# Kernel optimization log

Measured on AMD Instinct MI355X. Metric: run time of the kernel, lower is better.

Reference implementation:

```python
import jax, jax.numpy as jnp
import numpy as np

B, C, H, W = 4, 256, 64, 64
HEADS, GROUPS = 8, 8
HEAD_DIM = C // HEADS
EPS_GN = 1e-5
EPS_NORM = 1e-12


def group_norm(x, gamma, beta):
    b, c, h, w = x.shape
    xr = x.reshape(b, GROUPS, c // GROUPS, h, w)
    mean = xr.mean(axis=(2, 3, 4), keepdims=True)
    var = xr.var(axis=(2, 3, 4), keepdims=True)
    xn = ((xr - mean) / jnp.sqrt(var + EPS_GN)).reshape(b, c, h, w)
    return xn * gamma[None, :, None, None] + beta[None, :, None, None]


def conv1x1(x, w):
    # w: (C_out, C_in) pointwise conv
    return jnp.einsum('oc,bchw->bohw', w, x)


def dwconv3x3(x, w, b):
    # depthwise 3x3, w: (C, 1, 3, 3)
    y = jax.lax.conv_general_dilated(
        x, w, window_strides=(1, 1), padding='SAME',
        dimension_numbers=('NCHW', 'OIHW', 'NCHW'),
        feature_group_count=C)
    return y + b[None, :, None, None]


def setup_inputs() -> dict:
    key = jax.random.key(0)
    ks = jax.random.split(key, 7)
    s = 0.05
    f32 = jnp.float32
    return {
        'x': jax.random.normal(ks[0], (B, C, H, W), f32),
        'wq': jax.random.normal(ks[1], (C, C), f32) * s,
        'gq_gamma': jnp.ones((C,), f32), 'gq_beta': jnp.zeros((C,), f32),
        'wk': jax.random.normal(ks[2], (C, C), f32) * s,
        'gk_gamma': jnp.ones((C,), f32), 'gk_beta': jnp.zeros((C,), f32),
        'wv': jax.random.normal(ks[3], (C, C), f32) * s,
        'wp': jax.random.normal(ks[4], (C, C), f32) * s,
        'bp': jnp.zeros((C,), f32),
        'gp_gamma': jnp.ones((C,), f32), 'gp_beta': jnp.zeros((C,), f32),
        'dw1': jax.random.normal(ks[5], (C, 1, 3, 3), f32) * s,
        'db1': jnp.zeros((C,), f32),
        'dw2': jax.random.normal(ks[6], (C, 1, 3, 3), f32) * s,
        'db2': jnp.zeros((C,), f32),
    }


def reference(x, wq, gq_gamma, gq_beta, wk, gk_gamma, gk_beta, wv,
              wp, bp, gp_gamma, gp_beta, dw1, db1, dw2, db2):
    b, c, h, w = x.shape
    q = group_norm(conv1x1(x, wq), gq_gamma, gq_beta)
    k = group_norm(conv1x1(x, wk), gk_gamma, gk_beta)
    v = conv1x1(x, wv)

    def to_tokens(t):
        # (B,C,H,W) -> (B*H*W, heads, head_dim)
        return t.transpose(0, 2, 3, 1).reshape(b * h * w, HEADS, HEAD_DIM)

    q, k, v = to_tokens(q), to_tokens(k), to_tokens(v)
    qn = q / jnp.maximum(jnp.linalg.norm(q, axis=-1, keepdims=True), EPS_NORM)
    kn = k / jnp.maximum(jnp.linalg.norm(k, axis=-1, keepdims=True), EPS_NORM)
    scale = 1.0 / np.sqrt(HEAD_DIM).astype(np.float32)
    # per-pixel spectral attention: (N, heads, d, d)
    attn = jnp.einsum('nhd,nhe->nhde', qn, kn) * scale
    attn = jax.nn.softmax(attn, axis=-1)
    out = jnp.einsum('nhde,nhe->nhd', attn, v)
    out = out.reshape(b, h, w, c).transpose(0, 3, 1, 2)

    pos = dwconv3x3(x, dw1, db1)
    pos = jax.nn.gelu(pos, approximate=False)
    pos = dwconv3x3(pos, dw2, db2)

    out = out + pos
    out = conv1x1(out, wp) + bp[None, :, None, None]
    out = group_norm(out, gp_gamma, gp_beta)
    return out
```

## Files before the change

### kernel.cpp

```cpp
#include <hip/hip_runtime.h>
#include <math.h>
#include <stdint.h>

#define C_ 256
#define HW_ 4096
#define PLANE (C_*HW_)
#define INV_CNT (1.f / 131072.f)
#define NSLOT 16

typedef __attribute__((ext_vector_type(8))) short bf16x8;
typedef __attribute__((ext_vector_type(4))) float f32x4;

__device__ __forceinline__ unsigned short f2bf(float f) {
    union { float f; unsigned int u; } v; v.f = f;
    unsigned int r = v.u + 0x7fffu + ((v.u >> 16) & 1u);
    return (unsigned short)(r >> 16);
}

__device__ __forceinline__ float bf2f(unsigned short u) {
    return __uint_as_float(((unsigned)u) << 16);
}

__device__ __forceinline__ void load_lds16(const void* g, void* l) {
    __builtin_amdgcn_global_load_lds(
        (const __attribute__((address_space(1))) unsigned int*)g,
        (__attribute__((address_space(3))) unsigned int*)l, 16, 0, 0);
}

__global__ __launch_bounds__(256) void transpose_cvt_kernel(
    const float* __restrict__ src, unsigned short* __restrict__ dst,
    const float* __restrict__ wq, const float* __restrict__ wk,
    const float* __restrict__ wv, const float* __restrict__ wp,
    unsigned short* __restrict__ wbf, float* __restrict__ stats)
{
    __shared__ float tile[64][65];
    int t = threadIdx.x;

    int bid = blockIdx.x + 64 * (blockIdx.y + 4 * blockIdx.z);
    {
        int widx = bid * 256 + t;
        const float* s = (widx < 65536) ? wq : (widx < 131072) ? wk
                       : (widx < 196608) ? wv : wp;
        wbf[widx] = f2bf(s[widx & 65535]);
        if (bid == 0) {
#pragma unroll
            for (int i = 0; i < 12; i++) stats[t + i * 256] = 0.f;
        }
    }

    int b = blockIdx.z;
    const float* s = src + (size_t)b * PLANE;
    unsigned short* d = dst + (size_t)b * PLANE;
    int c0 = blockIdx.y * 64, n0 = blockIdx.x * 64;
    int r = t >> 6, col = t & 63;
#pragma unroll
    for (int i = 0; i < 16; i++)
        tile[r + i * 4][col] = s[(size_t)(c0 + r + i * 4) * HW_ + n0 + col];
    __syncthreads();
#pragma unroll
    for (int i = 0; i < 16; i++)
        d[(size_t)(n0 + r + i * 4) * 256 + c0 + col] = f2bf(tile[col][r + i * 4]);
}

__global__ __launch_bounds__(256) void transpose_cvt_add_kernel(
    const unsigned short* __restrict__ pos, const unsigned short* __restrict__ attn,
    unsigned short* __restrict__ dst)
{
    __shared__ float tile[64][65];
    int b = blockIdx.z;
    const unsigned short* s = pos + (size_t)b * PLANE;
    const unsigned short* a = attn + (size_t)b * PLANE;
    unsigned short* d = dst + (size_t)b * PLANE;
    int c0 = blockIdx.y * 64, n0 = blockIdx.x * 64;
    int t = threadIdx.x;
    int r = t >> 6, col = t & 63;
#pragma unroll
    for (int i = 0; i < 16; i++)
        tile[r + i * 4][col] = bf2f(s[(size_t)(c0 + r + i * 4) * HW_ + n0 + col]);
    __syncthreads();
#pragma unroll
    for (int i = 0; i < 16; i++) {
        size_t o = (size_t)(n0 + r + i * 4) * 256 + c0 + col;
        d[o] = f2bf(tile[col][r + i * 4] + bf2f(a[o]));
    }
}

__device__ __forceinline__ void mfma_core(
    const unsigned short* __restrict__ A,
    const unsigned short* __restrict__ Bm,
    int m0, int n0, f32x4 (&acc)[4][4],
    unsigned short* sA, unsigned short* sB)
{
    const int t = threadIdx.x;
    const int lane = t & 63, wave = t >> 6;

#pragma unroll
    for (int i = 0; i < 4; i++)
#pragma unroll
        for (int j = 0; j < 4; j++) acc[i][j] = (f32x4)0.f;

    const int srow = wave * 32 + (lane >> 2);
    const int scol = (lane & 3) * 8;
    const unsigned short* ga = A  + (size_t)(m0 + srow) * 256 + scol;
    const unsigned short* gb = Bm + (size_t)(n0 + srow) * 256 + scol;
    const int lbase = (wave * 32) * 32;

    const int wm = wave >> 1, wn = wave & 1;
    const int fr = lane & 15, kg = lane >> 4;

    for (int k0 = 0; k0 < 256; k0 += 64) {
        if (k0) __syncthreads();
        load_lds16(ga + k0,            sA + lbase);
        load_lds16(ga + k0 + 16 * 256, sA + lbase + 16 * 32);
        load_lds16(gb + k0,            sB + lbase);
        load_lds16(gb + k0 + 16 * 256, sB + lbase + 16 * 32);
        load_lds16(ga + k0 + 32,            sA + 4096 + lbase);
        load_lds16(ga + k0 + 32 + 16 * 256, sA + 4096 + lbase + 16 * 32);
        load_lds16(gb + k0 + 32,            sB + 4096 + lbase);
        load_lds16(gb + k0 + 32 + 16 * 256, sB + 4096 + lbase + 16 * 32);
        __syncthreads();

#pragma unroll
        for (int kk = 0; kk < 2; kk++) {
            bf16x8 af[4], bfr[4];
#pragma unroll
            for (int i = 0; i < 4; i++) {
                af[i]  = *(const bf16x8*)(sA + kk * 4096 + (wm * 64 + i * 16 + fr) * 32 + kg * 8);
                bfr[i] = *(const bf16x8*)(sB + kk * 4096 + (wn * 64 + i * 16 + fr) * 32 + kg * 8);
            }
#pragma unroll
            for (int mi = 0; mi < 4; mi++)
#pragma unroll
                for (int ni = 0; ni < 4; ni++)
                    acc[mi][ni] = __builtin_amdgcn_mfma_f32_16x16x32_bf16(
                        af[mi], bfr[ni], acc[mi][ni], 0, 0, 0);
        }
    }
}

__device__ __forceinline__ void stat_atomic(
    float s0, float ss0, float s1, float ss1, float* d0, float* d1)
{
#pragma unroll
    for (int off = 32; off >= 1; off >>= 1) {
        s0  += __shfl_down(s0, off);  ss0 += __shfl_down(ss0, off);
        s1  += __shfl_down(s1, off);  ss1 += __shfl_down(ss1, off);
    }
    if ((threadIdx.x & 63) == 0) {
        atomicAdd(d0, s0); atomicAdd(d0 + 1, ss0);
        atomicAdd(d1, s1); atomicAdd(d1 + 1, ss1);
    }
}

__device__ __forceinline__ void stat_read(const float* sp, float& S, float& SS) {
    S = 0.f; SS = 0.f;
#pragma unroll
    for (int i = 0; i < NSLOT; i++) { S += sp[i * 2]; SS += sp[i * 2 + 1]; }
}

__device__ __forceinline__ float gelu_exact(float v) {
    return 0.5f * v * (1.f + erff(v * 0.70710678118654752f));
}

__global__ __launch_bounds__(256) void gemm_qkv_dw_kernel(
    const unsigned short* __restrict__ wbf, const unsigned short* __restrict__ xT,
    unsigned short* __restrict__ q, unsigned short* __restrict__ k,
    unsigned short* __restrict__ v, float* __restrict__ stats,
    const float* __restrict__ x,
    const float* __restrict__ dw1, const float* __restrict__ db1,
    const float* __restrict__ dw2, const float* __restrict__ db2,
    unsigned short* __restrict__ pos)
{
    __shared__ __align__(16) char smem[66 * 68 * 4 * 2];
    const int bid = blockIdx.x;
    const int t = threadIdx.x;

    if (bid < 768) {
        unsigned short* sA = (unsigned short*)smem;
        unsigned short* sB = (unsigned short*)(smem + 16384);
        int z = bid >> 6, rr = bid & 63;
        int batch = z & 3, which = z >> 2;
        unsigned short* Y = ((which == 0) ? q : (which == 1) ? k : v)
                            + (size_t)batch * PLANE;
        const unsigned short* A  = wbf + which * 65536;
        const unsigned short* Bm = xT + (size_t)batch * PLANE;
        const int m0 = (rr & 1) * 128;
        const int n0 = (rr >> 1) * 128;

        f32x4 acc[4][4];
        mfma_core(A, Bm, m0, n0, acc, sA, sB);

        const int lane = t & 63, wave = t >> 6;
        const int wm = wave >> 1, wn = wave & 1;
        const int cl = lane & 15, qd = lane >> 4;

        if (which < 2) {
            float s[2] = {0.f, 0.f}, ss[2] = {0.f, 0.f};
#pragma unroll
            for (int mi = 0; mi < 4; mi++)
#pragma unroll
                for (int ni = 0; ni < 4; ni++)
#pragma unroll
                    for (int r = 0; r < 4; r++) {
                        float vv = acc[mi][ni][r];
                        s[mi >> 1] += vv; ss[mi >> 1] += vv * vv;
                    }
            int g0 = (m0 >> 5) + wm * 2;
            int slot = (rr >> 1) & (NSLOT - 1);
            float* d0 = stats + (size_t)(which * 32 + batch * 8 + g0) * (NSLOT * 2) + slot * 2;
            stat_atomic(s[0], ss[0], s[1], ss[1], d0, d0 + NSLOT * 2);
        }

#pragma unroll
        for (int mi = 0; mi < 4; mi++) {
            int oc = m0 + wm * 64 + mi * 16 + qd * 4;
#pragma unroll
            for (int ni = 0; ni < 4; ni++) {
                int token = n0 + wn * 64 + ni * 16 + cl;
                uint2 pk;
                pk.x = (unsigned)f2bf(acc[mi][ni][0]) | ((unsigned)f2bf(acc[mi][ni][1]) << 16);
                pk.y = (unsigned)f2bf(acc[mi][ni][2]) | ((unsigned)f2bf(acc[mi][ni][3]) << 16);
                *(uint2*)&Y[(size_t)token * 256 + oc] = pk;
            }
        }
    } else {
        float* xs = (float*)smem;
        float* ps = xs + 66 * 68;
        const int bc = bid - 768;
        const int c = bc & 255;
        const float* plane = x + (size_t)bc * 4096;

        float w1[9], w2[9];
#pragma unroll
        for (int i = 0; i < 9; i++) { w1[i] = dw1[c * 9 + i]; w2[i] = dw2[c * 9 + i]; }
        const float b1 = db1[c], b2 = db2[c];

        for (int i = t; i < 66 * 66; i += 256) {
            int r = i / 66, cc = i - r * 66;
            int gr = r - 1, gc = cc - 1;
            float vv = 0.f;
            if ((unsigned)gr < 64u && (unsigned)gc < 64u) vv = plane[gr * 64 + gc];
            xs[r * 68 + cc] = vv;
        }
        __syncthreads();

        for (int i = t; i < 66 * 66; i += 256) {
            int pr = i / 66, pc = i - pr * 66;
            int gr = pr - 1, gc = pc - 1;
            float val = 0.f;
            if ((unsigned)gr < 64u && (unsigned)gc < 64u) {
                float s = b1;
#pragma unroll
                for (int ky = 0; ky < 3; ky++)
#pragma unroll
                    for (int kx = 0; kx < 3; kx++)
                        s += w1[ky * 3 + kx] * xs[(gr + ky) * 68 + (gc + kx)];
                val = gelu_exact(s);
            }
            ps[pr * 68 + pc] = val;
        }
        __syncthreads();

        for (int i = t; i < 4096; i += 256) {
            int orow = i >> 6, ocol = i & 63;
            float s = b2;
#pragma unroll
            for (int ky = 0; ky < 3; ky++)
#pragma unroll
                for (int kx = 0; kx < 3; kx++)
                    s += w2[ky * 3 + kx] * ps[(orow + ky) * 68 + (ocol + kx)];
            pos[(size_t)bc * 4096 + i] = f2bf(s);
        }
    }
}

__global__ __launch_bounds__(256) void gemm_out_mfma(
    const unsigned short* __restrict__ wbf, const unsigned short* __restrict__ aT,
    const float* __restrict__ bp, unsigned short* __restrict__ yb,
    float* __restrict__ stats)
{
    __shared__ __align__(16) unsigned short sA[2 * 128 * 32];
    __shared__ __align__(16) unsigned short sB[2 * 128 * 32];
    int batch = blockIdx.z;
    const unsigned short* A  = aT + (size_t)batch * PLANE;
    const unsigned short* Bm = wbf + 3 * 65536;
    unsigned short* Y = yb + (size_t)batch * PLANE;
    const int m0 = blockIdx.x * 128;
    const int n0 = blockIdx.y * 128;

    f32x4 acc[4][4];
    mfma_core(A, Bm, m0, n0, acc, sA, sB);

    const int lane = threadIdx.x & 63, wave = threadIdx.x >> 6;
    const int wm = wave >> 1, wn = wave & 1;
    const int cl = lane & 15, qd = lane >> 4;

    float s[2] = {0.f, 0.f}, ss[2] = {0.f, 0.f};
#pragma unroll
    for (int ni = 0; ni < 4; ni++) {
        int oc = n0 + wn * 64 + ni * 16 + cl;
        float bb = bp[oc];
#pragma unroll
        for (int mi = 0; mi < 4; mi++) {
            int tk = m0 + wm * 64 + mi * 16 + qd * 4;
            float4 o;
            o.x = acc[mi][ni][0] + bb; o.y = acc[mi][ni][1] + bb;
            o.z = acc[mi][ni][2] + bb; o.w = acc[mi][ni][3] + bb;
            s[ni >> 1] += o.x + o.y + o.z + o.w;
            ss[ni >> 1] += o.x * o.x + o.y * o.y + o.z * o.z + o.w * o.w;
            uint2 pk;
            pk.x = (unsigned)f2bf(o.x) | ((unsigned)f2bf(o.y) << 16);
            pk.y = (unsigned)f2bf(o.z) | ((unsigned)f2bf(o.w) << 16);
            *(uint2*)&Y[(size_t)oc * HW_ + tk] = pk;
        }
    }
    int g0 = (n0 >> 5) + wn * 2;
    int slot = blockIdx.x & (NSLOT - 1);
    float* d0 = stats + (size_t)(64 + batch * 8 + g0) * (NSLOT * 2) + slot * 2;
    stat_atomic(s[0], ss[0], s[1], ss[1], d0, d0 + NSLOT * 2);
}

__device__ __forceinline__ void bf16x32_load(const unsigned short* p, float* o) {
    const uint4* u4 = (const uint4*)p;
#pragma unroll
    for (int i = 0; i < 4; i++) {
        uint4 u = u4[i];
        o[i*8+0] = __uint_as_float(u.x << 16); o[i*8+1] = __uint_as_float(u.x & 0xffff0000u);
        o[i*8+2] = __uint_as_float(u.y << 16); o[i*8+3] = __uint_as_float(u.y & 0xffff0000u);
        o[i*8+4] = __uint_as_float(u.z << 16); o[i*8+5] = __uint_as_float(u.z & 0xffff0000u);
        o[i*8+6] = __uint_as_float(u.w << 16); o[i*8+7] = __uint_as_float(u.w & 0xffff0000u);
    }
}

__global__ __launch_bounds__(256) void attn_tok_kernel(
    const unsigned short* __restrict__ qtok, const unsigned short* __restrict__ ktok,
    const unsigned short* __restrict__ vtok, const float* __restrict__ stats,
    const float* __restrict__ gqg, const float* __restrict__ gqb,
    const float* __restrict__ gkg, const float* __restrict__ gkb,
    unsigned short* __restrict__ out)
{
    __shared__ float sqg[256], sqb[256], skg[256], skb[256];
    const int t = threadIdx.x;
    sqg[t] = gqg[t]; sqb[t] = gqb[t]; skg[t] = gkg[t]; skb[t] = gkb[t];
    __syncthreads();

    const int h = t & 7;
    const int pix = blockIdx.x * 32 + (t >> 3);
    const int b = pix >> 12;
    const size_t base = (size_t)pix * 256 + h * 32;
    const float K2 = 0.17677669529663687f * 1.4426950408889634f;

    float a[32], kn[32], vv[32];

    {
        float S, SS;
        stat_read(stats + (size_t)(b * 8 + h) * (NSLOT * 2), S, SS);
        float m = S * INV_CNT;
        float r = rsqrtf(SS * INV_CNT - m * m + 1e-5f);
        float qv[32], ssum = 0.f;
        bf16x32_load(qtok + base, qv);
#pragma unroll
        for (int j = 0; j < 32; j++) {
            float g = r * sqg[h * 32 + j];
            qv[j] = (qv[j] - m) * g + sqb[h * 32 + j];
            ssum = fmaf(qv[j], qv[j], ssum);
        }
        float inv = K2 / fmaxf(sqrtf(ssum), 1e-12f);
#pragma unroll
        for (int j = 0; j < 32; j++) a[j] = qv[j] * inv;
    }
    {
        float S, SS;
        stat_read(stats + (size_t)(32 + b * 8 + h) * (NSLOT * 2), S, SS);
        float m = S * INV_CNT;
        float r = rsqrtf(SS * INV_CNT - m * m + 1e-5f);
        float ssum = 0.f;
        bf16x32_load(ktok + base, kn);
#pragma unroll
        for (int j = 0; j < 32; j++) {
            float g = r * skg[h * 32 + j];
            kn[j] = (kn[j] - m) * g + skb[h * 32 + j];
            ssum = fmaf(kn[j], kn[j], ssum);
        }
        float inv = 1.f / fmaxf(sqrtf(ssum), 1e-12f);
#pragma unroll
        for (int j = 0; j < 32; j++) kn[j] *= inv;
    }
    bf16x32_load(vtok + base, vv);

    uint4* op = (uint4*)(out + base);
#pragma unroll
    for (int di = 0; di < 4; di++) {
        unsigned int od[4];
#pragma unroll
        for (int dp = 0; dp < 4; dp++) {
            float o2[2];
#pragma unroll
            for (int dd = 0; dd < 2; dd++) {
                float ad = a[di * 8 + dp * 2 + dd];
                float num = 0.f, den = 0.f;
#pragma unroll
                for (int e = 0; e < 32; e++) {
                    float w = __builtin_amdgcn_exp2f(ad * kn[e]);
                    num = fmaf(w, vv[e], num);
                    den += w;
                }
                o2[dd] = num / den;
            }
            od[dp] = (unsigned)f2bf(o2[0]) | ((unsigned)f2bf(o2[1]) << 16);
        }
        op[di] = make_uint4(od[0], od[1], od[2], od[3]);
    }
}

__global__ __launch_bounds__(256) void gn_apply_kernel(
    const unsigned short* __restrict__ src, float* __restrict__ y,
    const float* __restrict__ stats,
    const float* __restrict__ gamma, const float* __restrict__ beta)
{
    int i4 = blockIdx.x * 256 + threadIdx.x;
    int idx = i4 * 4;
    int c = (idx >> 12) & 255;
    int bg = ((idx >> 20) << 3) | (c >> 5);
    float S, SS;
    stat_read(stats + (size_t)(64 + bg) * (NSLOT * 2), S, SS);
    float mean = S * INV_CNT;
    float rstd = rsqrtf(SS * INV_CNT - mean * mean + 1e-5f);
    float ga = rstd * gamma[c], be = beta[c] - mean * ga;
    uint2 u = *(const uint2*)&src[idx];
    float4 v4;
    v4.x = bf2f((unsigned short)(u.x & 0xffff)) * ga + be;
    v4.y = bf2f((unsigned short)(u.x >> 16))    * ga + be;
    v4.z = bf2f((unsigned short)(u.y & 0xffff)) * ga + be;
    v4.w = bf2f((unsigned short)(u.y >> 16))    * ga + be;
    *(float4*)&y[idx] = v4;
}

extern "C" void kernel_launch(void* const* d_in, const int* in_sizes, int n_in,
                              void* d_out, int out_size, void* d_ws, size_t ws_size,
                              hipStream_t stream)
{
    const float* x   = (const float*)d_in[0];
    const float* wq  = (const float*)d_in[1];
    const float* gqg = (const float*)d_in[2];
    const float* gqb = (const float*)d_in[3];
    const float* wk  = (const float*)d_in[4];
    const float* gkg = (const float*)d_in[5];
    const float* gkb = (const float*)d_in[6];
    const float* wv  = (const float*)d_in[7];
    const float* wp  = (const float*)d_in[8];
    const float* bp  = (const float*)d_in[9];
    const float* gpg = (const float*)d_in[10];
    const float* gpb = (const float*)d_in[11];
    const float* dw1 = (const float*)d_in[12];
    const float* db1 = (const float*)d_in[13];
    const float* dw2 = (const float*)d_in[14];
    const float* db2 = (const float*)d_in[15];
    float* out = (float*)d_out;

    char* ws = (char*)d_ws;
    const size_t MB8 = (size_t)8 * 1024 * 1024;
    unsigned short* qtok = (unsigned short*)(ws);
    unsigned short* ktok = (unsigned short*)(ws + MB8);
    unsigned short* vtok = (unsigned short*)(ws + 2 * MB8);
    unsigned short* atok = (unsigned short*)(ws + 3 * MB8);
    unsigned short* xT   = (unsigned short*)(ws + 4 * MB8);
    unsigned short* aT   = xT;
    unsigned short* outb = ktok;
    unsigned short* wbf  = (unsigned short*)(ws + 5 * MB8);
    float*          stats= (float*)(ws + 5 * MB8 + 524288);
    unsigned short* pos  = (unsigned short*)(ws + 6 * MB8);

    dim3 blk(256);
    transpose_cvt_kernel<<<dim3(64, 4, 4), blk, 0, stream>>>(x, xT, wq, wk, wv, wp, wbf, stats);
    gemm_qkv_dw_kernel<<<dim3(1792), blk, 0, stream>>>(wbf, xT, qtok, ktok, vtok, stats,
                                                       x, dw1, db1, dw2, db2, pos);
    attn_tok_kernel<<<dim3(512), blk, 0, stream>>>(qtok, ktok, vtok, stats,
                                                   gqg, gqb, gkg, gkb, atok);
    transpose_cvt_add_kernel<<<dim3(64, 4, 4), blk, 0, stream>>>(pos, atok, aT);
    gemm_out_mfma<<<dim3(32, 2, 4), blk, 0, stream>>>(wbf, aT, bp, outb, stats);
    gn_apply_kernel<<<dim3(4096), blk, 0, stream>>>(outb, out, stats, gpg, gpb);
}
```

Before: 182.0 us.

## Fuse all stages into one cooperative persistent kernel with grid syncs

Replaces six separate kernel launches with a single cooperative persistent kernel that runs the weight conversion, transpose, depthwise conv, QKV GEMM, attention, output GEMM and group-norm apply as phases separated by grid.sync. The pos add is folded into the attention phase, which reads pos tiles through LDS, so the separate transpose-add pass and its intermediate buffer go away. The goal is to cut launch overhead and the extra memory round trips. In exchange, the grid is capped at a fixed occupancy-based size, grid-wide barriers are added, and the depthwise conv no longer overlaps with the QKV GEMM.

```diff
diff --git a/kernel.cpp b/kernel.cpp
--- a/kernel.cpp
+++ b/kernel.cpp
@@ -1,12 +1,16 @@
 #include <hip/hip_runtime.h>
+#include <hip/hip_cooperative_groups.h>
 #include <math.h>
 #include <stdint.h>
+
+namespace cg = cooperative_groups;
 
 #define C_ 256
 #define HW_ 4096
 #define PLANE (C_*HW_)
 #define INV_CNT (1.f / 131072.f)
 #define NSLOT 16
+#define PSTRIDE 264
 
 typedef __attribute__((ext_vector_type(8))) short bf16x8;
 typedef __attribute__((ext_vector_type(4))) float f32x4;
@@ -27,61 +31,15 @@
         (__attribute__((address_space(3))) unsigned int*)l, 16, 0, 0);
 }
 
-__global__ __launch_bounds__(256) void transpose_cvt_kernel(
-    const float* __restrict__ src, unsigned short* __restrict__ dst,
-    const float* __restrict__ wq, const float* __restrict__ wk,
-    const float* __restrict__ wv, const float* __restrict__ wp,
-    unsigned short* __restrict__ wbf, float* __restrict__ stats)
-{
-    __shared__ float tile[64][65];
-    int t = threadIdx.x;
-
-    int bid = blockIdx.x + 64 * (blockIdx.y + 4 * blockIdx.z);
-    {
-        int widx = bid * 256 + t;
-        const float* s = (widx < 65536) ? wq : (widx < 131072) ? wk
-                       : (widx < 196608) ? wv : wp;
-        wbf[widx] = f2bf(s[widx & 65535]);
-        if (bid == 0) {
-#pragma unroll
-            for (int i = 0; i < 12; i++) stats[t + i * 256] = 0.f;
-        }
-    }
-
-    int b = blockIdx.z;
-    const float* s = src + (size_t)b * PLANE;
-    unsigned short* d = dst + (size_t)b * PLANE;
-    int c0 = blockIdx.y * 64, n0 = blockIdx.x * 64;
-    int r = t >> 6, col = t & 63;
-#pragma unroll
-    for (int i = 0; i < 16; i++)
-        tile[r + i * 4][col] = s[(size_t)(c0 + r + i * 4) * HW_ + n0 + col];
-    __syncthreads();
-#pragma unroll
-    for (int i = 0; i < 16; i++)
-        d[(size_t)(n0 + r + i * 4) * 256 + c0 + col] = f2bf(tile[col][r + i * 4]);
-}
-
-__global__ __launch_bounds__(256) void transpose_cvt_add_kernel(
-    const unsigned short* __restrict__ pos, const unsigned short* __restrict__ attn,
-    unsigned short* __restrict__ dst)
-{
-    __shared__ float tile[64][65];
-    int b = blockIdx.z;
-    const unsigned short* s = pos + (size_t)b * PLANE;
-    const unsigned short* a = attn + (size_t)b * PLANE;
-    unsigned short* d = dst + (size_t)b * PLANE;
-    int c0 = blockIdx.y * 64, n0 = blockIdx.x * 64;
-    int t = threadIdx.x;
-    int r = t >> 6, col = t & 63;
-#pragma unroll
-    for (int i = 0; i < 16; i++)
-        tile[r + i * 4][col] = bf2f(s[(size_t)(c0 + r + i * 4) * HW_ + n0 + col]);
-    __syncthreads();
-#pragma unroll
-    for (int i = 0; i < 16; i++) {
-        size_t o = (size_t)(n0 + r + i * 4) * 256 + c0 + col;
-        d[o] = f2bf(tile[col][r + i * 4] + bf2f(a[o]));
+__device__ __forceinline__ void bf16x32_load(const unsigned short* p, float* o) {
+    const uint4* u4 = (const uint4*)p;
+#pragma unroll
+    for (int i = 0; i < 4; i++) {
+        uint4 u = u4[i];
+        o[i*8+0] = __uint_as_float(u.x << 16); o[i*8+1] = __uint_as_float(u.x & 0xffff0000u);
+        o[i*8+2] = __uint_as_float(u.y << 16); o[i*8+3] = __uint_as_float(u.y & 0xffff0000u);
+        o[i*8+4] = __uint_as_float(u.z << 16); o[i*8+5] = __uint_as_float(u.z & 0xffff0000u);
+        o[i*8+6] = __uint_as_float(u.w << 16); o[i*8+7] = __uint_as_float(u.w & 0xffff0000u);
     }
 }
 
@@ -162,322 +120,382 @@
     return 0.5f * v * (1.f + erff(v * 0.70710678118654752f));
 }
 
-__global__ __launch_bounds__(256) void gemm_qkv_dw_kernel(
-    const unsigned short* __restrict__ wbf, const unsigned short* __restrict__ xT,
-    unsigned short* __restrict__ q, unsigned short* __restrict__ k,
-    unsigned short* __restrict__ v, float* __restrict__ stats,
-    const float* __restrict__ x,
-    const float* __restrict__ dw1, const float* __restrict__ db1,
-    const float* __restrict__ dw2, const float* __restrict__ db2,
-    unsigned short* __restrict__ pos)
+struct MegaParams {
+    const float* x;
+    const float* wq; const float* wk; const float* wv; const float* wp;
+    const float* bp;
+    const float* gqg; const float* gqb; const float* gkg; const float* gkb;
+    const float* gpg; const float* gpb;
+    const float* dw1; const float* db1; const float* dw2; const float* db2;
+    unsigned short* xT;
+    unsigned short* wbf;
+    unsigned short* qtok; unsigned short* ktok; unsigned short* vtok;
+    unsigned short* pos;
+    float* stats;
+    float* out;
+};
+
+__global__ __launch_bounds__(256, 3) void mega_kernel(MegaParams P)
 {
     __shared__ __align__(16) char smem[66 * 68 * 4 * 2];
+    cg::grid_group grid = cg::this_grid();
     const int bid = blockIdx.x;
+    const int NBg = gridDim.x;
     const int t = threadIdx.x;
 
-    if (bid < 768) {
+    {
+        float (*tile)[65] = (float(*)[65])smem;
+        for (int u = bid; u < 1024; u += NBg) {
+            int widx = u * 256 + t;
+            const float* wsrc = (widx < 65536) ? P.wq : (widx < 131072) ? P.wk
+                              : (widx < 196608) ? P.wv : P.wp;
+            P.wbf[widx] = f2bf(wsrc[widx & 65535]);
+            if (u == 0) {
+#pragma unroll
+                for (int i = 0; i < 12; i++) P.stats[t + i * 256] = 0.f;
+            }
+            int b = u >> 8, c0 = ((u >> 6) & 3) * 64, n0 = (u & 63) * 64;
+            const float* s = P.x + (size_t)b * PLANE;
+            unsigned short* d = P.xT + (size_t)b * PLANE;
+            int r = t >> 6, col = t & 63;
+            __syncthreads();
+#pragma unroll
+            for (int i = 0; i < 16; i++)
+                tile[r + i * 4][col] = s[(size_t)(c0 + r + i * 4) * HW_ + n0 + col];
+            __syncthreads();
+#pragma unroll
+            for (int i = 0; i < 16; i++)
+                d[(size_t)(n0 + r + i * 4) * 256 + c0 + col] = f2bf(tile[col][r + i * 4]);
+        }
+    }
+
+    {
+        float* xs = (float*)smem;
+        float* ps = xs + 66 * 68;
+        for (int u = bid; u < 1024; u += NBg) {
+            int c = u & 255;
+            const float* plane = P.x + (size_t)u * 4096;
+            float w1[9], w2[9];
+#pragma unroll
+            for (int i = 0; i < 9; i++) { w1[i] = P.dw1[c * 9 + i]; w2[i] = P.dw2[c * 9 + i]; }
+            const float b1 = P.db1[c], b2 = P.db2[c];
+            __syncthreads();
+            for (int i = t; i < 66 * 66; i += 256) {
+                int r = i / 66, cc = i - r * 66;
+                int gr = r - 1, gc = cc - 1;
+                float v = 0.f;
+                if ((unsigned)gr < 64u && (unsigned)gc < 64u) v = plane[gr * 64 + gc];
+                xs[r * 68 + cc] = v;
+            }
+            __syncthreads();
+            for (int i = t; i < 66 * 66; i += 256) {
+                int pr = i / 66, pc = i - pr * 66;
+                int gr = pr - 1, gc = pc - 1;
+                float val = 0.f;
+                if ((unsigned)gr < 64u && (unsigned)gc < 64u) {
+                    float s = b1;
+#pragma unroll
+                    for (int ky = 0; ky < 3; ky++)
+#pragma unroll
+                        for (int kx = 0; kx < 3; kx++)
+                            s += w1[ky * 3 + kx] * xs[(gr + ky) * 68 + (gc + kx)];
+                    val = gelu_exact(s);
+                }
+                ps[pr * 68 + pc] = val;
+            }
+            __syncthreads();
+            for (int i = t; i < 4096; i += 256) {
+                int orow = i >> 6, ocol = i & 63;
+                float s = b2;
+#pragma unroll
+                for (int ky = 0; ky < 3; ky++)
+#pragma unroll
+                    for (int kx = 0; kx < 3; kx++)
+                        s += w2[ky * 3 + kx] * ps[(orow + ky) * 68 + (ocol + kx)];
+                P.pos[(size_t)u * 4096 + i] = f2bf(s);
+            }
+        }
+    }
+
+    grid.sync();
+
+    {
         unsigned short* sA = (unsigned short*)smem;
         unsigned short* sB = (unsigned short*)(smem + 16384);
-        int z = bid >> 6, rr = bid & 63;
-        int batch = z & 3, which = z >> 2;
-        unsigned short* Y = ((which == 0) ? q : (which == 1) ? k : v)
-                            + (size_t)batch * PLANE;
-        const unsigned short* A  = wbf + which * 65536;
-        const unsigned short* Bm = xT + (size_t)batch * PLANE;
-        const int m0 = (rr & 1) * 128;
-        const int n0 = (rr >> 1) * 128;
-
-        f32x4 acc[4][4];
-        mfma_core(A, Bm, m0, n0, acc, sA, sB);
-
-        const int lane = t & 63, wave = t >> 6;
-        const int wm = wave >> 1, wn = wave & 1;
-        const int cl = lane & 15, qd = lane >> 4;
-
-        if (which < 2) {
+        for (int u = bid; u < 768; u += NBg) {
+            int z = u >> 6, rr = u & 63;
+            int batch = z & 3, which = z >> 2;
+            unsigned short* Y = ((which == 0) ? P.qtok : (which == 1) ? P.ktok : P.vtok)
+                                + (size_t)batch * PLANE;
+            const unsigned short* A  = P.wbf + which * 65536;
+            const unsigned short* Bm = P.xT + (size_t)batch * PLANE;
+            const int m0 = (rr & 1) * 128;
+            const int n0 = (rr >> 1) * 128;
+
+            __syncthreads();
+            f32x4 acc[4][4];
+            mfma_core(A, Bm, m0, n0, acc, sA, sB);
+
+            const int lane = t & 63, wave = t >> 6;
+            const int wm = wave >> 1, wn = wave & 1;
+            const int cl = lane & 15, qd = lane >> 4;
+
+            if (which < 2) {
+                float s[2] = {0.f, 0.f}, ss[2] = {0.f, 0.f};
+#pragma unroll
+                for (int mi = 0; mi < 4; mi++)
+#pragma unroll
+                    for (int ni = 0; ni < 4; ni++)
+#pragma unroll
+                        for (int r = 0; r < 4; r++) {
+                            float vv = acc[mi][ni][r];
+                            s[mi >> 1] += vv; ss[mi >> 1] += vv * vv;
+                        }
+                int g0 = (m0 >> 5) + wm * 2;
+                int slot = (rr >> 1) & (NSLOT - 1);
+                float* d0 = P.stats + (size_t)(which * 32 + batch * 8 + g0) * (NSLOT * 2) + slot * 2;
+                stat_atomic(s[0], ss[0], s[1], ss[1], d0, d0 + NSLOT * 2);
+            }
+
+#pragma unroll
+            for (int mi = 0; mi < 4; mi++) {
+                int oc = m0 + wm * 64 + mi * 16 + qd * 4;
+#pragma unroll
+                for (int ni = 0; ni < 4; ni++) {
+                    int token = n0 + wn * 64 + ni * 16 + cl;
+                    uint2 pk;
+                    pk.x = (unsigned)f2bf(acc[mi][ni][0]) | ((unsigned)f2bf(acc[mi][ni][1]) << 16);
+                    pk.y = (unsigned)f2bf(acc[mi][ni][2]) | ((unsigned)f2bf(acc[mi][ni][3]) << 16);
+                    *(uint2*)&Y[(size_t)token * 256 + oc] = pk;
+                }
+            }
+        }
+    }
+
+    grid.sync();
+
+    {
+        float* sqg = (float*)smem;
+        float* sqb = sqg + 256;
+        float* skg = sqg + 512;
+        float* skb = sqg + 768;
+        unsigned short* ptile = (unsigned short*)(smem + 4096);
+        unsigned short* aT = P.xT;
+        sqg[t] = P.gqg[t]; sqb[t] = P.gqb[t]; skg[t] = P.gkg[t]; skb[t] = P.gkb[t];
+
+        const float K2 = 0.17677669529663687f * 1.4426950408889634f;
+        const int h = t & 7;
+        const int p = t >> 3;
+
+        for (int u = bid; u < 512; u += NBg) {
+            const int pix0 = u * 32;
+            const int b = pix0 >> 12;
+            const int n0 = pix0 & 4095;
+            __syncthreads();
+            {
+                const uint4* prow = (const uint4*)(P.pos + (size_t)b * PLANE + (size_t)t * HW_ + n0);
+#pragma unroll
+                for (int i = 0; i < 4; i++) {
+                    uint4 uu = prow[i];
+                    ptile[(i*8+0) * PSTRIDE + t] = (unsigned short)(uu.x & 0xffff);
+                    ptile[(i*8+1) * PSTRIDE + t] = (unsigned short)(uu.x >> 16);
+                    ptile[(i*8+2) * PSTRIDE + t] = (unsigned short)(uu.y & 0xffff);
+                    ptile[(i*8+3) * PSTRIDE + t] = (unsigned short)(uu.y >> 16);
+                    ptile[(i*8+4) * PSTRIDE + t] = (unsigned short)(uu.z & 0xffff);
+                    ptile[(i*8+5) * PSTRIDE + t] = (unsigned short)(uu.z >> 16);
+                    ptile[(i*8+6) * PSTRIDE + t] = (unsigned short)(uu.w & 0xffff);
+                    ptile[(i*8+7) * PSTRIDE + t] = (unsigned short)(uu.w >> 16);
+                }
+            }
+            __syncthreads();
+
+            const int pix = pix0 + p;
+            const size_t base = (size_t)pix * 256 + h * 32;
+            float a[32], kn[32], vv[32];
+
+            {
+                float S, SS;
+                stat_read(P.stats + (size_t)(b * 8 + h) * (NSLOT * 2), S, SS);
+                float m = S * INV_CNT;
+                float r = rsqrtf(SS * INV_CNT - m * m + 1e-5f);
+                float qv[32], ssum = 0.f;
+                bf16x32_load(P.qtok + base, qv);
+#pragma unroll
+                for (int j = 0; j < 32; j++) {
+                    float g = r * sqg[h * 32 + j];
+                    qv[j] = (qv[j] - m) * g + sqb[h * 32 + j];
+                    ssum = fmaf(qv[j], qv[j], ssum);
+                }
+                float inv = K2 / fmaxf(sqrtf(ssum), 1e-12f);
+#pragma unroll
+                for (int j = 0; j < 32; j++) a[j] = qv[j] * inv;
+            }
+            {
+                float S, SS;
+                stat_read(P.stats + (size_t)(32 + b * 8 + h) * (NSLOT * 2), S, SS);
+                float m = S * INV_CNT;
+                float r = rsqrtf(SS * INV_CNT - m * m + 1e-5f);
+                float ssum = 0.f;
+                bf16x32_load(P.ktok + base, kn);
+#pragma unroll
+                for (int j = 0; j < 32; j++) {
+                    float g = r * skg[h * 32 + j];
+                    kn[j] = (kn[j] - m) * g + skb[h * 32 + j];
+                    ssum = fmaf(kn[j], kn[j], ssum);
+                }
+                float inv = 1.f / fmaxf(sqrtf(ssum), 1e-12f);
+#pragma unroll
+                for (int j = 0; j < 32; j++) kn[j] *= inv;
+            }
+            bf16x32_load(P.vtok + base, vv);
+
+            const unsigned short* pl = ptile + p * PSTRIDE + h * 32;
+            uint4* op = (uint4*)(aT + base);
+#pragma unroll
+            for (int di = 0; di < 4; di++) {
+                uint4 up = *(const uint4*)(pl + di * 8);
+                float pv8[8];
+                pv8[0] = bf2f((unsigned short)(up.x & 0xffff)); pv8[1] = bf2f((unsigned short)(up.x >> 16));
+                pv8[2] = bf2f((unsigned short)(up.y & 0xffff)); pv8[3] = bf2f((unsigned short)(up.y >> 16));
+                pv8[4] = bf2f((unsigned short)(up.z & 0xffff)); pv8[5] = bf2f((unsigned short)(up.z >> 16));
+                pv8[6] = bf2f((unsigned short)(up.w & 0xffff)); pv8[7] = bf2f((unsigned short)(up.w >> 16));
+                unsigned int od[4];
+#pragma unroll
+                for (int dp = 0; dp < 4; dp++) {
+                    float o2[2];
+#pragma unroll
+                    for (int dd = 0; dd < 2; dd++) {
+                        float ad = a[di * 8 + dp * 2 + dd];
+                        float num = 0.f, den = 0.f;
+#pragma unroll
+                        for (int e = 0; e < 32; e++) {
+                            float w = __builtin_amdgcn_exp2f(ad * kn[e]);
+                            num = fmaf(w, vv[e], num);
+                            den += w;
+                        }
+                        o2[dd] = num / den + pv8[dp * 2 + dd];
+                    }
+                    od[dp] = (unsigned)f2bf(o2[0]) | ((unsigned)f2bf(o2[1]) << 16);
+                }
+                op[di] = make_uint4(od[0], od[1], od[2], od[3]);
+            }
+        }
+    }
+
+    grid.sync();
+
+    {
+        unsigned short* sA = (unsigned short*)smem;
+        unsigned short* sB = (unsigned short*)(smem + 16384);
+        const unsigned short* aT = P.xT;
+        unsigned short* outb = P.ktok;
+        for (int u = bid; u < 256; u += NBg) {
+            int bx = u & 31, z2 = u >> 5;
+            int ny = z2 & 1, batch = z2 >> 1;
+            const unsigned short* A  = aT + (size_t)batch * PLANE;
+            const unsigned short* Bm = P.wbf + 3 * 65536;
+            unsigned short* Y = outb + (size_t)batch * PLANE;
+            const int m0 = bx * 128;
+            const int n0 = ny * 128;
+
+            __syncthreads();
+            f32x4 acc[4][4];
+            mfma_core(A, Bm, m0, n0, acc, sA, sB);
+
+            const int lane = t & 63, wave = t >> 6;
+            const int wm = wave >> 1, wn = wave & 1;
+            const int cl = lane & 15, qd = lane >> 4;
+
             float s[2] = {0.f, 0.f}, ss[2] = {0.f, 0.f};
 #pragma unroll
-            for (int mi = 0; mi < 4; mi++)
-#pragma unroll
-                for (int ni = 0; ni < 4; ni++)
-#pragma unroll
-                    for (int r = 0; r < 4; r++) {
-                        float vv = acc[mi][ni][r];
-                        s[mi >> 1] += vv; ss[mi >> 1] += vv * vv;
-                    }
-            int g0 = (m0 >> 5) + wm * 2;
-            int slot = (rr >> 1) & (NSLOT - 1);
-            float* d0 = stats + (size_t)(which * 32 + batch * 8 + g0) * (NSLOT * 2) + slot * 2;
+            for (int ni = 0; ni < 4; ni++) {
+                int oc = n0 + wn * 64 + ni * 16 + cl;
+                float bb = P.bp[oc];
+#pragma unroll
+                for (int mi = 0; mi < 4; mi++) {
+                    int tk = m0 + wm * 64 + mi * 16 + qd * 4;
+                    float4 o;
+                    o.x = acc[mi][ni][0] + bb; o.y = acc[mi][ni][1] + bb;
+                    o.z = acc[mi][ni][2] + bb; o.w = acc[mi][ni][3] + bb;
+                    s[ni >> 1] += o.x + o.y + o.z + o.w;
+                    ss[ni >> 1] += o.x * o.x + o.y * o.y + o.z * o.z + o.w * o.w;
+                    uint2 pk;
+                    pk.x = (unsigned)f2bf(o.x) | ((unsigned)f2bf(o.y) << 16);
+                    pk.y = (unsigned)f2bf(o.z) | ((unsigned)f2bf(o.w) << 16);
+                    *(uint2*)&Y[(size_t)oc * HW_ + tk] = pk;
+                }
+            }
+            int g0 = (n0 >> 5) + wn * 2;
+            int slot = bx & (NSLOT - 1);
+            float* d0 = P.stats + (size_t)(64 + batch * 8 + g0) * (NSLOT * 2) + slot * 2;
             stat_atomic(s[0], ss[0], s[1], ss[1], d0, d0 + NSLOT * 2);
         }
-
-#pragma unroll
-        for (int mi = 0; mi < 4; mi++) {
-            int oc = m0 + wm * 64 + mi * 16 + qd * 4;
-#pragma unroll
-            for (int ni = 0; ni < 4; ni++) {
-                int token = n0 + wn * 64 + ni * 16 + cl;
-                uint2 pk;
-                pk.x = (unsigned)f2bf(acc[mi][ni][0]) | ((unsigned)f2bf(acc[mi][ni][1]) << 16);
-                pk.y = (unsigned)f2bf(acc[mi][ni][2]) | ((unsigned)f2bf(acc[mi][ni][3]) << 16);
-                *(uint2*)&Y[(size_t)token * 256 + oc] = pk;
-            }
-        }
-    } else {
-        float* xs = (float*)smem;
-        float* ps = xs + 66 * 68;
-        const int bc = bid - 768;
-        const int c = bc & 255;
-        const float* plane = x + (size_t)bc * 4096;
-
-        float w1[9], w2[9];
-#pragma unroll
-        for (int i = 0; i < 9; i++) { w1[i] = dw1[c * 9 + i]; w2[i] = dw2[c * 9 + i]; }
-        const float b1 = db1[c], b2 = db2[c];
-
-        for (int i = t; i < 66 * 66; i += 256) {
-            int r = i / 66, cc = i - r * 66;
-            int gr = r - 1, gc = cc - 1;
-            float vv = 0.f;
-            if ((unsigned)gr < 64u && (unsigned)gc < 64u) vv = plane[gr * 64 + gc];
-            xs[r * 68 + cc] = vv;
-        }
-        __syncthreads();
-
-        for (int i = t; i < 66 * 66; i += 256) {
-            int pr = i / 66, pc = i - pr * 66;
-            int gr = pr - 1, gc = pc - 1;
-            float val = 0.f;
-            if ((unsigned)gr < 64u && (unsigned)gc < 64u) {
-                float s = b1;
-#pragma unroll
-                for (int ky = 0; ky < 3; ky++)
-#pragma unroll
-                    for (int kx = 0; kx < 3; kx++)
-                        s += w1[ky * 3 + kx] * xs[(gr + ky) * 68 + (gc + kx)];
-                val = gelu_exact(s);
-            }
-            ps[pr * 68 + pc] = val;
-        }
-        __syncthreads();
-
-        for (int i = t; i < 4096; i += 256) {
-            int orow = i >> 6, ocol = i & 63;
-            float s = b2;
-#pragma unroll
-            for (int ky = 0; ky < 3; ky++)
-#pragma unroll
-                for (int kx = 0; kx < 3; kx++)
-                    s += w2[ky * 3 + kx] * ps[(orow + ky) * 68 + (ocol + kx)];
-            pos[(size_t)bc * 4096 + i] = f2bf(s);
-        }
-    }
-}
-
-__global__ __launch_bounds__(256) void gemm_out_mfma(
-    const unsigned short* __restrict__ wbf, const unsigned short* __restrict__ aT,
-    const float* __restrict__ bp, unsigned short* __restrict__ yb,
-    float* __restrict__ stats)
-{
-    __shared__ __align__(16) unsigned short sA[2 * 128 * 32];
-    __shared__ __align__(16) unsigned short sB[2 * 128 * 32];
-    int batch = blockIdx.z;
-    const unsigned short* A  = aT + (size_t)batch * PLANE;
-    const unsigned short* Bm = wbf + 3 * 65536;
-    unsigned short* Y = yb + (size_t)batch * PLANE;
-    const int m0 = blockIdx.x * 128;
-    const int n0 = blockIdx.y * 128;
-
-    f32x4 acc[4][4];
-    mfma_core(A, Bm, m0, n0, acc, sA, sB);
-
-    const int lane = threadIdx.x & 63, wave = threadIdx.x >> 6;
-    const int wm = wave >> 1, wn = wave & 1;
-    const int cl = lane & 15, qd = lane >> 4;
-
-    float s[2] = {0.f, 0.f}, ss[2] = {0.f, 0.f};
-#pragma unroll
-    for (int ni = 0; ni < 4; ni++) {
-        int oc = n0 + wn * 64 + ni * 16 + cl;
-        float bb = bp[oc];
-#pragma unroll
-        for (int mi = 0; mi < 4; mi++) {
-            int tk = m0 + wm * 64 + mi * 16 + qd * 4;
-            float4 o;
-            o.x = acc[mi][ni][0] + bb; o.y = acc[mi][ni][1] + bb;
-            o.z = acc[mi][ni][2] + bb; o.w = acc[mi][ni][3] + bb;
-            s[ni >> 1] += o.x + o.y + o.z + o.w;
-            ss[ni >> 1] += o.x * o.x + o.y * o.y + o.z * o.z + o.w * o.w;
-            uint2 pk;
-            pk.x = (unsigned)f2bf(o.x) | ((unsigned)f2bf(o.y) << 16);
-            pk.y = (unsigned)f2bf(o.z) | ((unsigned)f2bf(o.w) << 16);
-            *(uint2*)&Y[(size_t)oc * HW_ + tk] = pk;
-        }
-    }
-    int g0 = (n0 >> 5) + wn * 2;
-    int slot = blockIdx.x & (NSLOT - 1);
-    float* d0 = stats + (size_t)(64 + batch * 8 + g0) * (NSLOT * 2) + slot * 2;
-    stat_atomic(s[0], ss[0], s[1], ss[1], d0, d0 + NSLOT * 2);
-}
-
-__device__ __forceinline__ void bf16x32_load(const unsigned short* p, float* o) {
-    const uint4* u4 = (const uint4*)p;
-#pragma unroll
-    for (int i = 0; i < 4; i++) {
-        uint4 u = u4[i];
-        o[i*8+0] = __uint_as_float(u.x << 16); o[i*8+1] = __uint_as_float(u.x & 0xffff0000u);
-        o[i*8+2] = __uint_as_float(u.y << 16); o[i*8+3] = __uint_as_float(u.y & 0xffff0000u);
-        o[i*8+4] = __uint_as_float(u.z << 16); o[i*8+5] = __uint_as_float(u.z & 0xffff0000u);
-        o[i*8+6] = __uint_as_float(u.w << 16); o[i*8+7] = __uint_as_float(u.w & 0xffff0000u);
-    }
-}
-
-__global__ __launch_bounds__(256) void attn_tok_kernel(
-    const unsigned short* __restrict__ qtok, const unsigned short* __restrict__ ktok,
-    const unsigned short* __restrict__ vtok, const float* __restrict__ stats,
-    const float* __restrict__ gqg, const float* __restrict__ gqb,
-    const float* __restrict__ gkg, const float* __restrict__ gkb,
-    unsigned short* __restrict__ out)
-{
-    __shared__ float sqg[256], sqb[256], skg[256], skb[256];
-    const int t = threadIdx.x;
-    sqg[t] = gqg[t]; sqb[t] = gqb[t]; skg[t] = gkg[t]; skb[t] = gkb[t];
-    __syncthreads();
-
-    const int h = t & 7;
-    const int pix = blockIdx.x * 32 + (t >> 3);
-    const int b = pix >> 12;
-    const size_t base = (size_t)pix * 256 + h * 32;
-    const float K2 = 0.17677669529663687f * 1.4426950408889634f;
-
-    float a[32], kn[32], vv[32];
+    }
+
+    grid.sync();
 
     {
-        float S, SS;
-        stat_read(stats + (size_t)(b * 8 + h) * (NSLOT * 2), S, SS);
-        float m = S * INV_CNT;
-        float r = rsqrtf(SS * INV_CNT - m * m + 1e-5f);
-        float qv[32], ssum = 0.f;
-        bf16x32_load(qtok + base, qv);
-#pragma unroll
-        for (int j = 0; j < 32; j++) {
-            float g = r * sqg[h * 32 + j];
-            qv[j] = (qv[j] - m) * g + sqb[h * 32 + j];
-            ssum = fmaf(qv[j], qv[j], ssum);
-        }
-        float inv = K2 / fmaxf(sqrtf(ssum), 1e-12f);
-#pragma unroll
-        for (int j = 0; j < 32; j++) a[j] = qv[j] * inv;
-    }
-    {
-        float S, SS;
-        stat_read(stats + (size_t)(32 + b * 8 + h) * (NSLOT * 2), S, SS);
-        float m = S * INV_CNT;
-        float r = rsqrtf(SS * INV_CNT - m * m + 1e-5f);
-        float ssum = 0.f;
-        bf16x32_load(ktok + base, kn);
-#pragma unroll
-        for (int j = 0; j < 32; j++) {
-            float g = r * skg[h * 32 + j];
-            kn[j] = (kn[j] - m) * g + skb[h * 32 + j];
-            ssum = fmaf(kn[j], kn[j], ssum);
-        }
-        float inv = 1.f / fmaxf(sqrtf(ssum), 1e-12f);
-#pragma unroll
-        for (int j = 0; j < 32; j++) kn[j] *= inv;
-    }
-    bf16x32_load(vtok + base, vv);
-
-    uint4* op = (uint4*)(out + base);
-#pragma unroll
-    for (int di = 0; di < 4; di++) {
-        unsigned int od[4];
-#pragma unroll
-        for (int dp = 0; dp < 4; dp++) {
-            float o2[2];
-#pragma unroll
-            for (int dd = 0; dd < 2; dd++) {
-                float ad = a[di * 8 + dp * 2 + dd];
-                float num = 0.f, den = 0.f;
-#pragma unroll
-                for (int e = 0; e < 32; e++) {
-                    float w = __builtin_amdgcn_exp2f(ad * kn[e]);
-                    num = fmaf(w, vv[e], num);
-                    den += w;
-                }
-                o2[dd] = num / den;
-            }
-            od[dp] = (unsigned)f2bf(o2[0]) | ((unsigned)f2bf(o2[1]) << 16);
-        }
-        op[di] = make_uint4(od[0], od[1], od[2], od[3]);
-    }
-}
-
-__global__ __launch_bounds__(256) void gn_apply_kernel(
-    const unsigned short* __restrict__ src, float* __restrict__ y,
-    const float* __restrict__ stats,
-    const float* __restrict__ gamma, const float* __restrict__ beta)
-{
-    int i4 = blockIdx.x * 256 + threadIdx.x;
-    int idx = i4 * 4;
-    int c = (idx >> 12) & 255;
-    int bg = ((idx >> 20) << 3) | (c >> 5);
-    float S, SS;
-    stat_read(stats + (size_t)(64 + bg) * (NSLOT * 2), S, SS);
-    float mean = S * INV_CNT;
-    float rstd = rsqrtf(SS * INV_CNT - mean * mean + 1e-5f);
-    float ga = rstd * gamma[c], be = beta[c] - mean * ga;
-    uint2 u = *(const uint2*)&src[idx];
-    float4 v4;
-    v4.x = bf2f((unsigned short)(u.x & 0xffff)) * ga + be;
-    v4.y = bf2f((unsigned short)(u.x >> 16))    * ga + be;
-    v4.z = bf2f((unsigned short)(u.y & 0xffff)) * ga + be;
-    v4.w = bf2f((unsigned short)(u.y >> 16))    * ga + be;
-    *(float4*)&y[idx] = v4;
+        const unsigned short* src = P.ktok;
+        for (int i4 = bid * 256 + t; i4 < 1048576; i4 += NBg * 256) {
+            int idx = i4 * 4;
+            int c = (idx >> 12) & 255;
+            int bg = ((idx >> 20) << 3) | (c >> 5);
+            float S, SS;
+            stat_read(P.stats + (size_t)(64 + bg) * (NSLOT * 2), S, SS);
+            float mean = S * INV_CNT;
+            float rstd = rsqrtf(SS * INV_CNT - mean * mean + 1e-5f);
+            float ga = rstd * P.gpg[c], be = P.gpb[c] - mean * ga;
+            uint2 u = *(const uint2*)&src[idx];
+            float4 v4;
+            v4.x = bf2f((unsigned short)(u.x & 0xffff)) * ga + be;
+            v4.y = bf2f((unsigned short)(u.x >> 16))    * ga + be;
+            v4.z = bf2f((unsigned short)(u.y & 0xffff)) * ga + be;
+            v4.w = bf2f((unsigned short)(u.y >> 16))    * ga + be;
+            *(float4*)&P.out[idx] = v4;
+        }
+    }
 }
 
 extern "C" void kernel_launch(void* const* d_in, const int* in_sizes, int n_in,
                               void* d_out, int out_size, void* d_ws, size_t ws_size,
                               hipStream_t stream)
 {
-    const float* x   = (const float*)d_in[0];
-    const float* wq  = (const float*)d_in[1];
-    const float* gqg = (const float*)d_in[2];
-    const float* gqb = (const float*)d_in[3];
-    const float* wk  = (const float*)d_in[4];
-    const float* gkg = (const float*)d_in[5];
-    const float* gkb = (const float*)d_in[6];
-    const float* wv  = (const float*)d_in[7];
-    const float* wp  = (const float*)d_in[8];
-    const float* bp  = (const float*)d_in[9];
-    const float* gpg = (const float*)d_in[10];
-    const float* gpb = (const float*)d_in[11];
-    const float* dw1 = (const float*)d_in[12];
-    const float* db1 = (const float*)d_in[13];
-    const float* dw2 = (const float*)d_in[14];
-    const float* db2 = (const float*)d_in[15];
-    float* out = (float*)d_out;
-
     char* ws = (char*)d_ws;
     const size_t MB8 = (size_t)8 * 1024 * 1024;
-    unsigned short* qtok = (unsigned short*)(ws);
-    unsigned short* ktok = (unsigned short*)(ws + MB8);
-    unsigned short* vtok = (unsigned short*)(ws + 2 * MB8);
-    unsigned short* atok = (unsigned short*)(ws + 3 * MB8);
-    unsigned short* xT   = (unsigned short*)(ws + 4 * MB8);
-    unsigned short* aT   = xT;
-    unsigned short* outb = ktok;
-    unsigned short* wbf  = (unsigned short*)(ws + 5 * MB8);
-    float*          stats= (float*)(ws + 5 * MB8 + 524288);
-    unsigned short* pos  = (unsigned short*)(ws + 6 * MB8);
-
-    dim3 blk(256);
-    transpose_cvt_kernel<<<dim3(64, 4, 4), blk, 0, stream>>>(x, xT, wq, wk, wv, wp, wbf, stats);
-    gemm_qkv_dw_kernel<<<dim3(1792), blk, 0, stream>>>(wbf, xT, qtok, ktok, vtok, stats,
-                                                       x, dw1, db1, dw2, db2, pos);
-    attn_tok_kernel<<<dim3(512), blk, 0, stream>>>(qtok, ktok, vtok, stats,
-                                                   gqg, gqb, gkg, gkb, atok);
-    transpose_cvt_add_kernel<<<dim3(64, 4, 4), blk, 0, stream>>>(pos, atok, aT);
-    gemm_out_mfma<<<dim3(32, 2, 4), blk, 0, stream>>>(wbf, aT, bp, outb, stats);
-    gn_apply_kernel<<<dim3(4096), blk, 0, stream>>>(outb, out, stats, gpg, gpb);
-}
+
+    MegaParams P;
+    P.x   = (const float*)d_in[0];
+    P.wq  = (const float*)d_in[1];
+    P.gqg = (const float*)d_in[2];
+    P.gqb = (const float*)d_in[3];
+    P.wk  = (const float*)d_in[4];
+    P.gkg = (const float*)d_in[5];
+    P.gkb = (const float*)d_in[6];
+    P.wv  = (const float*)d_in[7];
+    P.wp  = (const float*)d_in[8];
+    P.bp  = (const float*)d_in[9];
+    P.gpg = (const float*)d_in[10];
+    P.gpb = (const float*)d_in[11];
+    P.dw1 = (const float*)d_in[12];
+    P.db1 = (const float*)d_in[13];
+    P.dw2 = (const float*)d_in[14];
+    P.db2 = (const float*)d_in[15];
+    P.qtok = (unsigned short*)(ws);
+    P.ktok = (unsigned short*)(ws + MB8);
+    P.vtok = (unsigned short*)(ws + 2 * MB8);
+    P.xT   = (unsigned short*)(ws + 3 * MB8);
+    P.pos  = (unsigned short*)(ws + 4 * MB8);
+    P.wbf  = (unsigned short*)(ws + 5 * MB8);
+    P.stats= (float*)(ws + 5 * MB8 + 524288);
+    P.out  = (float*)d_out;
+
+    int occ = 0;
+    if (hipOccupancyMaxActiveBlocksPerMultiprocessor(&occ, mega_kernel, 256, 0)
+        != hipSuccess || occ <= 0) occ = 3;
+    int nb = occ * 256;
+    if (nb > 768) nb = 768;
+
+    void* args[] = { (void*)&P };
+    hipLaunchCooperativeKernel((const void*)mega_kernel, dim3(nb), dim3(256),
+                               args, 0, stream);
+}
```

New measurement: 453.5 us. 2.49x slower.
